# Kernel tuning notes

Hardware: AMD Instinct MI355X
Metric: run time of the kernel (lower is better)

The kernel has to match this reference:

```python
import jax, jax.numpy as jnp
import numpy as np

DIM = 512
HEADS = 8
FOCAL_LEVEL = 2  # depthwise kernel sizes: 3, 5 (focal_factor*k + focal_window)
LN_EPS = 1e-5


def _ln(x, w, b):
    m = jnp.mean(x, axis=-1, keepdims=True)
    v = jnp.var(x, axis=-1, keepdims=True)
    return (x - m) / jnp.sqrt(v + LN_EPS) * w + b


def _dwconv(x, w):
    # x: (B, C, H, W), w: (C, 1, k, k) depthwise, SAME padding (odd kernels)
    return jax.lax.conv_general_dilated(
        x, w, window_strides=(1, 1), padding='SAME',
        feature_group_count=x.shape[1],
        dimension_numbers=('NCHW', 'OIHW', 'NCHW'))


def setup_inputs() -> dict:
    key = jax.random.key(0)
    ks = jax.random.split(key, 16)
    B, Nl, H, W, d = 16, 512, 32, 32, DIM
    L = FOCAL_LEVEL
    p = lambda i, shape, s=0.02: (jax.random.normal(ks[i], shape, jnp.float32) * s)
    return {
        'latents': jax.random.normal(ks[0], (B, Nl, d), jnp.float32),
        'context': jax.random.normal(ks[1], (B, H * W, d), jnp.float32),
        'H': H, 'W': W,
        'norm_l_w': jnp.ones((d,), jnp.float32), 'norm_l_b': jnp.zeros((d,), jnp.float32),
        'norm_c_w': jnp.ones((d,), jnp.float32), 'norm_c_b': jnp.zeros((d,), jnp.float32),
        'norm2_w': jnp.ones((d,), jnp.float32), 'norm2_b': jnp.zeros((d,), jnp.float32),
        'Wq': p(2, (d, d)), 'Wk': p(3, (d, d)),
        'Wf': p(4, (d, d + L + 1)), 'bf': jnp.zeros((d + L + 1,), jnp.float32),
        'fk0': p(5, (d, 1, 3, 3), 0.1), 'fk1': p(6, (d, 1, 5, 5), 0.1),
        'h_w': p(7, (d, d)), 'h_b': jnp.zeros((d,), jnp.float32),
        'Wproj': p(8, (d, d)), 'bproj': jnp.zeros((d,), jnp.float32),
        'fc1_w': p(9, (d, 4 * d)), 'fc1_b': jnp.zeros((4 * d,), jnp.float32),
        'fc2_w': p(10, (4 * d, d)), 'fc2_b': jnp.zeros((d,), jnp.float32),
    }


def reference(latents, context, H, W,
              norm_l_w, norm_l_b, norm_c_w, norm_c_b, norm2_w, norm2_b,
              Wq, Wk, Wf, bf, fk0, fk1, h_w, h_b, Wproj, bproj,
              fc1_w, fc1_b, fc2_w, fc2_b):
    B, Nl, C = latents.shape
    Nc = context.shape[1]
    hd = C // HEADS
    scale = hd ** -0.5
    L = FOCAL_LEVEL
    gelu = lambda x: jax.nn.gelu(x, approximate=False)  # torch nn.GELU default

    xl = _ln(latents, norm_l_w, norm_l_b)
    xc = _ln(context, norm_c_w, norm_c_b)

    # cross attention scores
    q = (xl @ Wq).reshape(B, Nl, HEADS, hd)
    k = (xc @ Wk).reshape(B, Nc, HEADS, hd)
    attn = jax.nn.softmax(jnp.einsum('bqhd,bkhd->bhqk', q, k) * scale, axis=-1)

    # focal modulation on the context to build V
    f = (xc @ Wf + bf).reshape(B, H, W, C + L + 1).transpose(0, 3, 1, 2)  # (B, C+L+1, H, W)
    v_ctx = f[:, :C]
    gates = f[:, C:]
    acc = jnp.zeros_like(v_ctx)
    for l, w in enumerate((fk0, fk1)):  # sequential multi-scale depthwise convs
        v_ctx = gelu(_dwconv(v_ctx, w))
        acc = acc + v_ctx * gates[:, l:l + 1]
    g = gelu(jnp.mean(v_ctx, axis=(2, 3), keepdims=True))  # global branch
    acc = acc + g * gates[:, L:L + 1]

    # 1x1 conv modulator h
    mod = jnp.einsum('bihw,io->bohw', acc, h_w) + h_b[None, :, None, None]
    v = mod.reshape(B, C, Nc).transpose(0, 2, 1).reshape(B, Nc, HEADS, hd)

    y = jnp.einsum('bhqk,bkhd->bqhd', attn, v).reshape(B, Nl, C) @ Wproj + bproj
    latents = latents + y
    h2 = _ln(latents, norm2_w, norm2_b)
    latents = latents + (gelu(h2 @ fc1_w + fc1_b) @ fc2_w + fc2_b)
    return latents
```

## Files before the change

kernel.cpp:

```cpp
#include <hip/hip_runtime.h>
#include <hip/hip_bf16.h>
#include <math.h>

#define NB 16
#define NLAT 512
#define NCTX 1024
#define CD 512
#define NH 8
#define HD 64

typedef unsigned short ushort_t;
typedef __attribute__((ext_vector_type(8))) __bf16 bf16x8;
typedef __attribute__((ext_vector_type(8))) unsigned short u16x8;
typedef __attribute__((ext_vector_type(4))) unsigned short u16x4;
typedef __attribute__((ext_vector_type(4))) float f32x4;
typedef __attribute__((ext_vector_type(2))) unsigned int u32x2;

__device__ __forceinline__ float bf2f(unsigned short u) {
  return __uint_as_float(((unsigned int)u) << 16);
}
__device__ __forceinline__ unsigned short f2bf(float f) {
  unsigned int x = __float_as_uint(f);
  return (unsigned short)((x + 0x7fffu + ((x >> 16) & 1u)) >> 16);
}
__device__ __forceinline__ float gelu_f(float x) {
  return 0.5f * x * (1.f + erff(x * 0.70710678118654752f));
}

typedef const __attribute__((address_space(1))) unsigned int* gptr1;
typedef __attribute__((address_space(3))) unsigned int* lptr3;
__device__ __forceinline__ void gload16(const void* g, void* l) {
  __builtin_amdgcn_global_load_lds((gptr1)g, (lptr3)l, 16, 0, 0);
}
__device__ __forceinline__ u32x2 tr64(unsigned a) {
  u32x2 d;
  asm volatile("ds_read_b64_tr_b16 %0, %1" : "=v"(d) : "v"(a));
  return d;
}
__device__ __forceinline__ void gload16_asm(const void* g, unsigned lds_uniform_base) {
  unsigned sb = __builtin_amdgcn_readfirstlane(lds_uniform_base);
  asm volatile("s_mov_b32 m0, %0\n"
               "global_load_lds_dwordx4 %1, off"
               :: "s"(sb), "v"(g) : "memory");
}
template<int N> __device__ __forceinline__ void vmwait() {
  if constexpr (N == 0)       asm volatile("s_waitcnt vmcnt(0)" ::: "memory");
  else if constexpr (N == 2)  asm volatile("s_waitcnt vmcnt(2)" ::: "memory");
  else if constexpr (N == 3)  asm volatile("s_waitcnt vmcnt(3)" ::: "memory");
  else if constexpr (N == 4)  asm volatile("s_waitcnt vmcnt(4)" ::: "memory");
  else if constexpr (N == 6)  asm volatile("s_waitcnt vmcnt(6)" ::: "memory");
  else if constexpr (N == 8)  asm volatile("s_waitcnt vmcnt(8)" ::: "memory");
  else if constexpr (N == 9)  asm volatile("s_waitcnt vmcnt(9)" ::: "memory");
}

__global__ __launch_bounds__(256)
void wprep(const float* __restrict__ Wq, const float* __restrict__ Wk,
           const float* __restrict__ Wf, const float* __restrict__ hw_,
           const float* __restrict__ Wp, const float* __restrict__ f1,
           const float* __restrict__ f2, const float* __restrict__ bfv,
           ushort_t* __restrict__ WqT, ushort_t* __restrict__ WkT,
           ushort_t* __restrict__ WfT, ushort_t* __restrict__ hwT,
           ushort_t* __restrict__ WpT, ushort_t* __restrict__ fc1T,
           ushort_t* __restrict__ fc2T, float* __restrict__ biaskf) {
  int b = blockIdx.x;
  if (b >= 3344) {
    int i = threadIdx.x;
#pragma unroll
    for (int j = 0; j < 4; j++) {
      int idx = j * 256 + i;
      biaskf[idx] = (idx < 512) ? 0.f : bfv[idx - 512];
    }
    return;
  }
  const float* W; ushort_t* WT; int K, N, tile;
  if (b < 256)       { W = Wq;  WT = WqT;  K = 512;  N = 512;  tile = b; }
  else if (b < 512)  { W = Wk;  WT = WkT;  K = 512;  N = 512;  tile = b - 256; }
  else if (b < 784)  { W = Wf;  WT = WfT;  K = 512;  N = 515;  tile = b - 512; }
  else if (b < 1040) { W = hw_; WT = hwT;  K = 512;  N = 512;  tile = b - 784; }
  else if (b < 1296) { W = Wp;  WT = WpT;  K = 512;  N = 512;  tile = b - 1040; }
  else if (b < 2320) { W = f1;  WT = fc1T; K = 512;  N = 2048; tile = b - 1296; }
  else               { W = f2;  WT = fc2T; K = 2048; N = 512;  tile = b - 2320; }
  int Kt = K >> 5;
  int kb = (tile % Kt) * 32, nb = (tile / Kt) * 32;
  __shared__ float ts[32][33];
  int tx = threadIdx.x & 31, ty = threadIdx.x >> 5;
  for (int i = ty; i < 32; i += 8) {
    int k = kb + i, n = nb + tx;
    ts[i][tx] = (k < K && n < N) ? W[(size_t)k * N + n] : 0.f;
  }
  __syncthreads();
  for (int i = ty; i < 32; i += 8) {
    int n = nb + i, k = kb + tx;
    if (n < N && k < K) WT[(size_t)n * K + k] = f2bf(ts[tx][i]);
  }
}

__global__ __launch_bounds__(256)
void ln_kernel(const float* __restrict__ x, const float* __restrict__ gw,
               const float* __restrict__ gb, ushort_t* __restrict__ out, int nrows) {
  int row = blockIdx.x * 4 + (threadIdx.x >> 6);
  int lane = threadIdx.x & 63;
  const float4* xr = (const float4*)(x + (size_t)row * CD);
  float4 a = xr[lane * 2], b = xr[lane * 2 + 1];
  float s  = a.x + a.y + a.z + a.w + b.x + b.y + b.z + b.w;
  float s2 = a.x*a.x + a.y*a.y + a.z*a.z + a.w*a.w + b.x*b.x + b.y*b.y + b.z*b.z + b.w*b.w;
  for (int off = 32; off; off >>= 1) { s += __shfl_xor(s, off); s2 += __shfl_xor(s2, off); }
  float mean = s * (1.f / CD);
  float inv = rsqrtf(s2 * (1.f / CD) - mean * mean + 1e-5f);
  const float4* wv = (const float4*)gw;
  const float4* bv = (const float4*)gb;
  float4 w0 = wv[lane*2], w1 = wv[lane*2+1], c0 = bv[lane*2], c1 = bv[lane*2+1];
  u16x8 o;
  o[0] = f2bf((a.x - mean) * inv * w0.x + c0.x);
  o[1] = f2bf((a.y - mean) * inv * w0.y + c0.y);
  o[2] = f2bf((a.z - mean) * inv * w0.z + c0.z);
  o[3] = f2bf((a.w - mean) * inv * w0.w + c0.w);
  o[4] = f2bf((b.x - mean) * inv * w1.x + c1.x);
  o[5] = f2bf((b.y - mean) * inv * w1.y + c1.y);
  o[6] = f2bf((b.z - mean) * inv * w1.z + c1.z);
  o[7] = f2bf((b.w - mean) * inv * w1.w + c1.w);
  *(u16x8*)(out + (size_t)row * CD + lane * 8) = o;
  (void)nrows;
}

template<int BM, int BN, int ACT_GELU, int HAS_BIAS, int HAS_RES, int OUT_BF16>
__global__ __launch_bounds__(256)
void gemm9(const ushort_t* __restrict__ A, const ushort_t* __restrict__ BT,
           const float* __restrict__ bias, const float* __restrict__ res,
           void* __restrict__ outp, int N, int K) {
  constexpr int TM = BM / 2, FM = TM / 16;
  constexpr int TN = BN / 2, FN = TN / 16;
  constexpr int LA = BM / 64, LB = BN / 64, L = LA + LB;
  constexpr int SLOT = (BM + BN) * 32;
  __shared__ __attribute__((aligned(16))) ushort_t SH[3][SLOT];

  const int t = threadIdx.x;
  const int lane = t & 63;
  const int wv = t >> 6;
  const int wr = wv >> 1, wc = wv & 1;
  const int g = lane >> 4, l15 = lane & 15;
  const int xsw = (g ^ ((l15 >> 1) & 3)) * 8;
  const size_t m0 = (size_t)blockIdx.x * BM;
  const size_t n0 = (size_t)blockIdx.y * BN;
  const int nK = K >> 5;

  f32x4 acc[FM][FN] = {};

  const ushort_t* Abase = A + m0 * K;
  const ushort_t* Bbase = BT + n0 * K;
  const unsigned shb = (unsigned)(size_t)(lptr3)&SH[0][0];
  const unsigned wofs = (unsigned)wv * 1024;

  auto stage = [&](int s, int kt) {
    const unsigned sb = shb + (unsigned)s * (SLOT * 2);
    const ushort_t* As = Abase + (size_t)kt * 32;
#pragma unroll
    for (int i = 0; i < LA; i++) {
      int li = i * 256 + t;
      int sc = ((li & 3) ^ ((li >> 3) & 3)) * 8;
      gload16_asm(As + (size_t)(li >> 2) * K + sc, sb + (unsigned)i * 4096 + wofs);
    }
    const ushort_t* Bs = Bbase + (size_t)kt * 32;
#pragma unroll
    for (int i = 0; i < LB; i++) {
      int li = i * 256 + t;
      int sc = ((li & 3) ^ ((li >> 3) & 3)) * 8;
      gload16_asm(Bs + (size_t)(li >> 2) * K + sc, sb + (unsigned)(BM * 64) + (unsigned)i * 4096 + wofs);
    }
  };

  auto compute = [&](int s) {
    const ushort_t* base = &SH[0][0] + s * SLOT;
    const ushort_t* Ab = base + wr * TM * 32;
    const ushort_t* Bb = base + BM * 32 + wc * TN * 32;
    bf16x8 Bf[FN], Af[FM];
#pragma unroll
    for (int n = 0; n < FN; n++)
      Bf[n] = *(const bf16x8*)(Bb + (n * 16 + l15) * 32 + xsw);
#pragma unroll
    for (int m = 0; m < FM; m++)
      Af[m] = *(const bf16x8*)(Ab + (m * 16 + l15) * 32 + xsw);
    __builtin_amdgcn_s_setprio(1);
#pragma unroll
    for (int m = 0; m < FM; m++)
#pragma unroll
      for (int n = 0; n < FN; n++)
        acc[m][n] = __builtin_amdgcn_mfma_f32_16x16x32_bf16(Af[m], Bf[n], acc[m][n], 0, 0, 0);
    __builtin_amdgcn_s_setprio(0);
  };

  stage(0, 0); stage(1, 1);
  for (int kt = 0; kt < nK; kt++) {
    int s = kt % 3;
    if (kt + 2 < nK) { stage((kt + 2) % 3, kt + 2); vmwait<2 * L>(); }
    else if (kt + 1 < nK) vmwait<L>();
    else vmwait<0>();
    __builtin_amdgcn_s_barrier();
    __builtin_amdgcn_sched_barrier(0);
    compute(s);
    __builtin_amdgcn_sched_barrier(0);
    __builtin_amdgcn_s_barrier();
  }

  const int colb = (int)n0 + wc * TN;
  float bv[FN];
#pragma unroll
  for (int n = 0; n < FN; n++) bv[n] = HAS_BIAS ? bias[colb + n * 16 + l15] : 0.f;

  if (OUT_BF16) {
    constexpr int ES = TN + 8;
    ushort_t* ep = &SH[0][0] + wv * (TM * ES);
#pragma unroll
    for (int m = 0; m < FM; m++)
#pragma unroll
      for (int n = 0; n < FN; n++)
#pragma unroll
        for (int r = 0; r < 4; r++) {
          float v = acc[m][n][r] + bv[n];
          if (ACT_GELU) v = gelu_f(v);
          ep[(m * 16 + g * 4 + r) * ES + n * 16 + l15] = f2bf(v);
        }
    asm volatile("s_waitcnt lgkmcnt(0)" ::: "memory");
    __builtin_amdgcn_sched_barrier(0);
    const size_t gr0 = m0 + wr * TM;
#pragma unroll
    for (int c = 0; c < TM * TN / 512; c++) {
      int idx = c * 512 + lane * 8;
      int lr = idx / TN, col = idx % TN;
      u16x8 vvv = *(const u16x8*)&ep[lr * ES + col];
      *(u16x8*)((ushort_t*)outp + (gr0 + lr) * N + colb + col) = vvv;
    }
  } else {
    const int rowb = (int)m0 + wr * TM + g * 4;
#pragma unroll
    for (int n = 0; n < FN; n++) {
      int col = colb + n * 16 + l15;
#pragma unroll
      for (int m = 0; m < FM; m++) {
#pragma unroll
        for (int r = 0; r < 4; r++) {
          size_t idx = (size_t)(rowb + m * 16 + r) * N + col;
          float v = acc[m][n][r] + bv[n];
          if (ACT_GELU) v = gelu_f(v);
          if (HAS_RES) v += res[idx];
          ((float*)outp)[idx] = v;
        }
      }
    }
  }
}

__global__ __launch_bounds__(256)
void gates_kernel(const ushort_t* __restrict__ xc, const ushort_t* __restrict__ WfT,
                  const float* __restrict__ bfv, float* __restrict__ gates) {
  int row = blockIdx.x * 4 + (threadIdx.x >> 6);
  int lane = threadIdx.x & 63;
  u16x8 xv = *(const u16x8*)(xc + (size_t)row * CD + lane * 8);
  float xf[8];
#pragma unroll
  for (int e = 0; e < 8; e++) xf[e] = bf2f(xv[e]);
  float sl[3];
#pragma unroll
  for (int l = 0; l < 3; l++) {
    u16x8 wvv = *(const u16x8*)(WfT + (size_t)(CD + l) * CD + lane * 8);
    float d = 0.f;
#pragma unroll
    for (int e = 0; e < 8; e++) d += xf[e] * bf2f(wvv[e]);
    for (int off = 32; off; off >>= 1) d += __shfl_xor(d, off);
    sl[l] = d;
  }
  if (lane == 0) {
    int b = row >> 10, p = row & 1023;
#pragma unroll
    for (int l = 0; l < 3; l++) gates[((size_t)b * 3 + l) * 1024 + p] = sl[l] + bfv[CD + l];
  }
}

__global__ __launch_bounds__(256)
void tr_bf16(const ushort_t* __restrict__ in, ushort_t* __restrict__ out, int R, int C,
             int irs, size_t ibs, size_t obs) {
  __shared__ ushort_t tile[64][72];
  size_t ibase = (size_t)blockIdx.z * ibs;
  size_t obase = (size_t)blockIdx.z * obs;
  int r0 = blockIdx.x * 64, c0 = blockIdx.y * 64;
  int t = threadIdx.x;
#pragma unroll
  for (int j = 0; j < 2; j++) {
    int lin = j * 256 + t;
    int r = lin >> 3, cc = (lin & 7) * 8;
    u16x8 v = *(const u16x8*)(in + ibase + (size_t)(r0 + r) * irs + c0 + cc);
#pragma unroll
    for (int e = 0; e < 8; e++) tile[r][cc + e] = v[e];
  }
  __syncthreads();
#pragma unroll
  for (int j = 0; j < 2; j++) {
    int lin = j * 256 + t;
    int c = lin >> 3, rr = (lin & 7) * 8;
    u16x8 v;
#pragma unroll
    for (int e = 0; e < 8; e++) v[e] = tile[rr + e][c];
    *(u16x8*)(out + obase + (size_t)(c0 + c) * R + r0 + rr) = v;
  }
}

__global__ __launch_bounds__(256)
void focal_conv(const ushort_t* __restrict__ ft, const float* __restrict__ gates,
                const float* __restrict__ fk0, const float* __restrict__ fk1,
                ushort_t* __restrict__ accc) {
  int bc = blockIdx.x;
  int b = bc >> 9, c = bc & 511;
  __shared__ float xs[34][37];
  __shared__ float vs[38][41];
  __shared__ float w0s[9], w1s[25];
  __shared__ float red[4];
  const int t = threadIdx.x;
  const int hh = t >> 3;
  const int w0c = (t & 7) * 4;

  float* xz = &xs[0][0];
  float* vz = &vs[0][0];
#pragma unroll
  for (int i = 0; i < 5; i++) { int idx = t + i * 256; if (idx < 34 * 37) xz[idx] = 0.f; }
#pragma unroll
  for (int i = 0; i < 7; i++) { int idx = t + i * 256; if (idx < 38 * 41) vz[idx] = 0.f; }
  if (t < 9)  w0s[t] = fk0[c * 9 + t];
  if (t < 25) w1s[t] = fk1[c * 25 + t];

  u16x4 vin = *(const u16x4*)(ft + (size_t)bc * 1024 + t * 4);
  const float* g0 = gates + (size_t)b * 3 * 1024;
  float4 ga = *(const float4*)(g0 + t * 4);
  float4 gb = *(const float4*)(g0 + 1024 + t * 4);
  float4 gc = *(const float4*)(g0 + 2048 + t * 4);
  __syncthreads();
#pragma unroll
  for (int j = 0; j < 4; j++) xs[hh + 1][w0c + 1 + j] = bf2f(vin[j]);
  __syncthreads();

  float accv[4];
  const float* gav = (const float*)&ga;
  const float* gbv = (const float*)&gb;
  const float* gcv = (const float*)&gc;
#pragma unroll
  for (int j = 0; j < 4; j++) {
    int ww = w0c + j;
    float s = 0.f;
#pragma unroll
    for (int dh = 0; dh < 3; dh++)
#pragma unroll
      for (int dw = 0; dw < 3; dw++)
        s += xs[hh + dh][ww + dw] * w0s[dh * 3 + dw];
    float v1 = gelu_f(s);
    vs[hh + 2][ww + 2] = v1;
    accv[j] = v1 * gav[j];
  }
  __syncthreads();

  float psum = 0.f;
#pragma unroll
  for (int j = 0; j < 4; j++) {
    int ww = w0c + j;
    float s = 0.f;
#pragma unroll
    for (int dh = 0; dh < 5; dh++)
#pragma unroll
      for (int dw = 0; dw < 5; dw++)
        s += vs[hh + dh][ww + dw] * w1s[dh * 5 + dw];
    float v2 = gelu_f(s);
    psum += v2;
    accv[j] += v2 * gbv[j];
  }
  for (int off = 32; off; off >>= 1) psum += __shfl_xor(psum, off);
  if ((t & 63) == 0) red[t >> 6] = psum;
  __syncthreads();
  float g = gelu_f((red[0] + red[1] + red[2] + red[3]) * (1.f / 1024.f));
  u16x4 o;
#pragma unroll
  for (int j = 0; j < 4; j++) o[j] = f2bf(accv[j] + g * gcv[j]);
  *(u16x4*)(accc + (size_t)bc * 1024 + t * 4) = o;
}

__global__ __launch_bounds__(512)
void flash_attn(const ushort_t* __restrict__ Q, const ushort_t* __restrict__ Kk,
                const ushort_t* __restrict__ V, ushort_t* __restrict__ Y, int kstride) {
  const int wg = blockIdx.x;
  const int swz = (wg & 7) * 64 + (wg >> 3);
  const int q0 = (swz & 3) * 128;
  const int h = (swz >> 2) & 7;
  const int b = swz >> 5;
  const int t = threadIdx.x, lane = t & 63, w = t >> 6;
  const int g = lane >> 4, l15 = lane & 15;
  __shared__ __attribute__((aligned(16))) ushort_t Ks[2][4096];
  __shared__ __attribute__((aligned(16))) ushort_t Vs[2][4096];
  __shared__ __attribute__((aligned(16))) ushort_t Ps[8][1024];

  const size_t qbase = (((size_t)b * NLAT) + q0 + w * 16 + l15) * CD + h * HD;
  bf16x8 aq[2];
#pragma unroll
  for (int kk = 0; kk < 2; kk++) {
    u16x8 u = *(const u16x8*)(Q + qbase + kk * 32 + g * 8);
    u16x8 o;
#pragma unroll
    for (int e = 0; e < 8; e++) o[e] = f2bf(bf2f(u[e]) * 0.125f);
    aq[kk] = *(bf16x8*)&o;
  }

  f32x4 accO[4] = {};
  float lsum[4] = {0.f, 0.f, 0.f, 0.f};
  const ushort_t* Kb = Kk + ((size_t)b * NCTX) * kstride + h * HD;
  const ushort_t* Vb = V  + ((size_t)b * NCTX) * CD + h * HD;
  const int krow = t >> 3;
  const int kseg = 8 * ((t & 7) ^ (krow & 7));
  const int vrow = (t >> 1) & 63;
  const int vcol = (t >> 7) * 16 + (t & 1) * 8;

  auto stage = [&](int buf, int kv) {
    const int k0 = kv * 64;
    gload16(Kb + (size_t)(k0 + krow) * kstride + kseg, &Ks[buf][t * 8]);
    gload16(Vb + (size_t)(k0 + vrow) * CD + vcol, &Vs[buf][t * 8]);
  };

  const unsigned vsbase0 = (unsigned)(size_t)(lptr3)&Vs[0][0];
  const unsigned vsbase1 = (unsigned)(size_t)(lptr3)&Vs[1][0];
  char* psb = (char*)&Ps[w][0];

  stage(0, 0);
  __syncthreads();
  int cur = 0;
  for (int kv = 0; kv < 16; kv++) {
    if (kv < 15) stage(cur ^ 1, kv + 1);

    const char* ksb = (const char*)&Ks[cur][0];
    f32x4 accS[4] = {};
#pragma unroll
    for (int kk = 0; kk < 2; kk++) {
#pragma unroll
      for (int n = 0; n < 4; n++) {
        int rr = n * 16 + l15;
        bf16x8 bk = *(const bf16x8*)(ksb + rr * 128 + ((kk * 64 + g * 16) ^ ((rr & 7) << 4)));
        accS[n] = __builtin_amdgcn_mfma_f32_16x16x32_bf16(aq[kk], bk, accS[n], 0, 0, 0);
      }
    }

#pragma unroll
    for (int n = 0; n < 4; n++)
#pragma unroll
      for (int r = 0; r < 4; r++) {
        float p = __expf(accS[n][r]);
        accS[n][r] = p;
        lsum[r] += p;
      }

#pragma unroll
    for (int n = 0; n < 4; n++)
#pragma unroll
      for (int r = 0; r < 4; r++) {
        int row = g * 4 + r;
        int cb = (n * 16 + l15) * 2;
        *(ushort_t*)(psb + row * 128 + (cb ^ ((row & 7) << 4))) = f2bf(accS[n][r]);
      }
    asm volatile("s_waitcnt lgkmcnt(0)" ::: "memory");
    __builtin_amdgcn_sched_barrier(0);
    bf16x8 ap0 = *(const bf16x8*)(psb + l15 * 128 + (((g * 16)) ^ ((l15 & 7) << 4)));
    bf16x8 ap1 = *(const bf16x8*)(psb + l15 * 128 + ((64 + g * 16) ^ ((l15 & 7) << 4)));

    const unsigned vsb = (cur ? vsbase1 : vsbase0) + g * 128;
    union PKU { u32x2 d2[2]; bf16x8 v; };
    PKU pk[8];
#pragma unroll
    for (int n = 0; n < 4; n++) {
      unsigned a = vsb + n * 2048;
      pk[n * 2].d2[0]     = tr64(a);
      pk[n * 2].d2[1]     = tr64(a + 128);
      pk[n * 2 + 1].d2[0] = tr64(a + 1024);
      pk[n * 2 + 1].d2[1] = tr64(a + 1152);
    }
    asm volatile("s_waitcnt lgkmcnt(0)" ::: "memory");
    __builtin_amdgcn_sched_barrier(0);
#pragma unroll
    for (int n = 0; n < 4; n++) {
      accO[n] = __builtin_amdgcn_mfma_f32_16x16x32_bf16(ap0, pk[n * 2].v, accO[n], 0, 0, 0);
      accO[n] = __builtin_amdgcn_mfma_f32_16x16x32_bf16(ap1, pk[n * 2 + 1].v, accO[n], 0, 0, 0);
    }
    __syncthreads();
    cur ^= 1;
  }

#pragma unroll
  for (int r = 0; r < 4; r++) {
    float s = lsum[r];
    s += __shfl_xor(s, 1); s += __shfl_xor(s, 2);
    s += __shfl_xor(s, 4); s += __shfl_xor(s, 8);
    lsum[r] = 1.f / s;
  }
#pragma unroll
  for (int n = 0; n < 4; n++) {
#pragma unroll
    for (int r = 0; r < 4; r++) {
      size_t row = q0 + w * 16 + g * 4 + r;
      size_t col = h * HD + n * 16 + l15;
      Y[(((size_t)b * NLAT) + row) * CD + col] = f2bf(accO[n][r] * lsum[r]);
    }
  }
}

extern "C" void kernel_launch(void* const* d_in, const int* in_sizes, int n_in,
                              void* d_out, int out_size, void* d_ws, size_t ws_size,
                              hipStream_t stream) {
  const float* latents  = (const float*)d_in[0];
  const float* context  = (const float*)d_in[1];
  const float* norm_l_w = (const float*)d_in[4];
  const float* norm_l_b = (const float*)d_in[5];
  const float* norm_c_w = (const float*)d_in[6];
  const float* norm_c_b = (const float*)d_in[7];
  const float* norm2_w  = (const float*)d_in[8];
  const float* norm2_b  = (const float*)d_in[9];
  const float* Wq    = (const float*)d_in[10];
  const float* Wk    = (const float*)d_in[11];
  const float* Wf    = (const float*)d_in[12];
  const float* bfv   = (const float*)d_in[13];
  const float* fk0   = (const float*)d_in[14];
  const float* fk1   = (const float*)d_in[15];
  const float* h_w   = (const float*)d_in[16];
  const float* h_b   = (const float*)d_in[17];
  const float* Wproj = (const float*)d_in[18];
  const float* bproj = (const float*)d_in[19];
  const float* fc1_w = (const float*)d_in[20];
  const float* fc1_b = (const float*)d_in[21];
  const float* fc2_w = (const float*)d_in[22];
  const float* fc2_b = (const float*)d_in[23];

  char* ws = (char*)d_ws;
  const size_t MB = 1024ull * 1024ull;
  ushort_t* WqT  = (ushort_t*)(ws + 0 * MB);
  ushort_t* WkT  = (ushort_t*)(ws + 1 * MB);
  ushort_t* WfT  = (ushort_t*)(ws + 1 * MB + 524288);
  ushort_t* hwT  = (ushort_t*)(ws + 3 * MB);
  ushort_t* WpT  = (ushort_t*)(ws + 4 * MB);
  ushort_t* fc1T = (ushort_t*)(ws + 5 * MB);
  ushort_t* fc2T = (ushort_t*)(ws + 7 * MB);
  float*    biaskf = (float*)(ws + 9 * MB);
  ushort_t* xl    = (ushort_t*)(ws + 10 * MB);
  ushort_t* xc    = (ushort_t*)(ws + 18 * MB);
  ushort_t* qb    = (ushort_t*)(ws + 34 * MB);
  ushort_t* kf    = (ushort_t*)(ws + 42 * MB);
  float*    gates = (float*)   (ws + 74 * MB);
  ushort_t* ftp   = (ushort_t*)(ws + 75 * MB);
  ushort_t* accc  = (ushort_t*)(ws + 91 * MB);
  ushort_t* acct  = (ushort_t*)(ws + 18 * MB);
  ushort_t* vb    = (ushort_t*)(ws + 75 * MB);
  ushort_t* yb    = (ushort_t*)(ws + 10 * MB);
  float*    lat1  = (float*)   (ws + 18 * MB);
  ushort_t* h2    = (ushort_t*)(ws + 34 * MB);
  ushort_t* a1    = (ushort_t*)(ws + 42 * MB);

  dim3 b256(256), b512(512);
  wprep<<<dim3(3345), b256, 0, stream>>>(Wq, Wk, Wf, h_w, Wproj, fc1_w, fc2_w, bfv,
                                         WqT, WkT, WfT, hwT, WpT, fc1T, fc2T, biaskf);
  ln_kernel<<<dim3(2048), b256, 0, stream>>>(latents, norm_l_w, norm_l_b, xl, 8192);
  ln_kernel<<<dim3(4096), b256, 0, stream>>>(context, norm_c_w, norm_c_b, xc, 16384);
  gemm9<128,64, 0,0,0,1><<<dim3(64, 8),   b256, 0, stream>>>(xl, WqT, nullptr, nullptr, qb, 512, 512);
  gemm9<128,64, 0,1,0,1><<<dim3(128, 16), b256, 0, stream>>>(xc, WkT, biaskf, nullptr, kf, 1024, 512);
  gates_kernel<<<dim3(4096), b256, 0, stream>>>(xc, WfT, bfv, gates);
  tr_bf16<<<dim3(16, 8, 16), b256, 0, stream>>>(kf + 512, ftp, 1024, 512, 1024, (size_t)1024*1024, (size_t)512*1024);
  focal_conv<<<dim3(8192), b256, 0, stream>>>(ftp, gates, fk0, fk1, accc);
  tr_bf16<<<dim3(8, 16, 16), b256, 0, stream>>>(accc, acct, 512, 1024, 1024, (size_t)512*1024, (size_t)1024*512);
  gemm9<128,64, 0,1,0,1><<<dim3(128, 8), b256, 0, stream>>>(acct, hwT, h_b, nullptr, vb, 512, 512);
  flash_attn<<<dim3(512), b512, 0, stream>>>(qb, kf, vb, yb, 1024);
  gemm9<128,64, 0,1,1,0><<<dim3(64, 8), b256, 0, stream>>>(yb, WpT, bproj, latents, lat1, 512, 512);
  ln_kernel<<<dim3(2048), b256, 0, stream>>>(lat1, norm2_w, norm2_b, h2, 8192);
  gemm9<128,64, 1,1,0,1><<<dim3(64, 32), b256, 0, stream>>>(h2, fc1T, fc1_b, nullptr, a1, 2048, 512);
  gemm9<128,64, 0,1,1,0><<<dim3(64, 8),  b256, 0, stream>>>(a1, fc2T, fc2_b, lat1, d_out, 512, 2048);
  (void)in_sizes; (void)n_in; (void)out_size; (void)ws_size;
}
```

Before: 238.3 us.

## Switch GEMMs to 64x64 tiles with 1D grid and XCD-aware block remap

Replaces the templated 128x64 GEMM with a fixed 64x64-tile kernel launched on a 1D grid. Block IDs are remapped so that consecutive tiles are grouped per XCD (bid&7 striding), which should improve L2 locality across the eight chiplets. Smaller tiles double the block count, giving more occupancy and better load balance across CUs, at the cost of lower per-block operand reuse and more global/LDS traffic per FLOP. Each stage now issues a single A and B load per thread.

```diff
diff --git a/kernel.cpp b/kernel.cpp
--- a/kernel.cpp
+++ b/kernel.cpp
@@ -37,20 +37,17 @@
   asm volatile("ds_read_b64_tr_b16 %0, %1" : "=v"(d) : "v"(a));
   return d;
 }
-__device__ __forceinline__ void gload16_asm(const void* g, unsigned lds_uniform_base) {
-  unsigned sb = __builtin_amdgcn_readfirstlane(lds_uniform_base);
+__device__ __forceinline__ void gload16_s(const void* g, unsigned sbase) {
   asm volatile("s_mov_b32 m0, %0\n"
                "global_load_lds_dwordx4 %1, off"
-               :: "s"(sb), "v"(g) : "memory");
+               :: "s"(sbase), "v"(g) : "memory");
 }
 template<int N> __device__ __forceinline__ void vmwait() {
   if constexpr (N == 0)       asm volatile("s_waitcnt vmcnt(0)" ::: "memory");
   else if constexpr (N == 2)  asm volatile("s_waitcnt vmcnt(2)" ::: "memory");
-  else if constexpr (N == 3)  asm volatile("s_waitcnt vmcnt(3)" ::: "memory");
   else if constexpr (N == 4)  asm volatile("s_waitcnt vmcnt(4)" ::: "memory");
   else if constexpr (N == 6)  asm volatile("s_waitcnt vmcnt(6)" ::: "memory");
   else if constexpr (N == 8)  asm volatile("s_waitcnt vmcnt(8)" ::: "memory");
-  else if constexpr (N == 9)  asm volatile("s_waitcnt vmcnt(9)" ::: "memory");
 }
 
 __global__ __launch_bounds__(256)
@@ -123,16 +120,19 @@
   (void)nrows;
 }
 
-template<int BM, int BN, int ACT_GELU, int HAS_BIAS, int HAS_RES, int OUT_BF16>
+template<int ACT_GELU, int HAS_BIAS, int HAS_RES, int OUT_BF16>
 __global__ __launch_bounds__(256)
-void gemm9(const ushort_t* __restrict__ A, const ushort_t* __restrict__ BT,
-           const float* __restrict__ bias, const float* __restrict__ res,
-           void* __restrict__ outp, int N, int K) {
-  constexpr int TM = BM / 2, FM = TM / 16;
-  constexpr int TN = BN / 2, FN = TN / 16;
-  constexpr int LA = BM / 64, LB = BN / 64, L = LA + LB;
-  constexpr int SLOT = (BM + BN) * 32;
+void gemm11(const ushort_t* __restrict__ A, const ushort_t* __restrict__ BT,
+            const float* __restrict__ bias, const float* __restrict__ res,
+            void* __restrict__ outp, int N, int K, int nN) {
+  constexpr int SLOT = 4096;
   __shared__ __attribute__((aligned(16))) ushort_t SH[3][SLOT];
+
+  const int bid = blockIdx.x;
+  const int q = gridDim.x >> 3;
+  const int lin = (bid & 7) * q + (bid >> 3);
+  const size_t m0 = (size_t)(lin / nN) * 64;
+  const size_t n0 = (size_t)(lin % nN) * 64;
 
   const int t = threadIdx.x;
   const int lane = t & 63;
@@ -140,51 +140,40 @@
   const int wr = wv >> 1, wc = wv & 1;
   const int g = lane >> 4, l15 = lane & 15;
   const int xsw = (g ^ ((l15 >> 1) & 3)) * 8;
-  const size_t m0 = (size_t)blockIdx.x * BM;
-  const size_t n0 = (size_t)blockIdx.y * BN;
   const int nK = K >> 5;
 
-  f32x4 acc[FM][FN] = {};
+  f32x4 acc[2][2] = {};
 
   const ushort_t* Abase = A + m0 * K;
   const ushort_t* Bbase = BT + n0 * K;
-  const unsigned shb = (unsigned)(size_t)(lptr3)&SH[0][0];
-  const unsigned wofs = (unsigned)wv * 1024;
+  const unsigned m0b = __builtin_amdgcn_readfirstlane(
+      (unsigned)(size_t)(lptr3)&SH[0][0] + (unsigned)wv * 1024u);
+
+  const int srow = t >> 2;
+  const int ssc = ((t & 3) ^ ((t >> 3) & 3)) * 8;
 
   auto stage = [&](int s, int kt) {
-    const unsigned sb = shb + (unsigned)s * (SLOT * 2);
-    const ushort_t* As = Abase + (size_t)kt * 32;
-#pragma unroll
-    for (int i = 0; i < LA; i++) {
-      int li = i * 256 + t;
-      int sc = ((li & 3) ^ ((li >> 3) & 3)) * 8;
-      gload16_asm(As + (size_t)(li >> 2) * K + sc, sb + (unsigned)i * 4096 + wofs);
-    }
-    const ushort_t* Bs = Bbase + (size_t)kt * 32;
-#pragma unroll
-    for (int i = 0; i < LB; i++) {
-      int li = i * 256 + t;
-      int sc = ((li & 3) ^ ((li >> 3) & 3)) * 8;
-      gload16_asm(Bs + (size_t)(li >> 2) * K + sc, sb + (unsigned)(BM * 64) + (unsigned)i * 4096 + wofs);
-    }
+    const unsigned sb = m0b + (unsigned)s * 8192u;
+    gload16_s(Abase + (size_t)srow * K + (size_t)kt * 32 + ssc, sb);
+    gload16_s(Bbase + (size_t)srow * K + (size_t)kt * 32 + ssc, sb + 4096u);
   };
 
   auto compute = [&](int s) {
     const ushort_t* base = &SH[0][0] + s * SLOT;
-    const ushort_t* Ab = base + wr * TM * 32;
-    const ushort_t* Bb = base + BM * 32 + wc * TN * 32;
-    bf16x8 Bf[FN], Af[FM];
-#pragma unroll
-    for (int n = 0; n < FN; n++)
+    const ushort_t* Ab = base + wr * (32 * 32);
+    const ushort_t* Bb = base + 64 * 32 + wc * (32 * 32);
+    bf16x8 Bf[2], Af[2];
+#pragma unroll
+    for (int n = 0; n < 2; n++)
       Bf[n] = *(const bf16x8*)(Bb + (n * 16 + l15) * 32 + xsw);
 #pragma unroll
-    for (int m = 0; m < FM; m++)
+    for (int m = 0; m < 2; m++)
       Af[m] = *(const bf16x8*)(Ab + (m * 16 + l15) * 32 + xsw);
     __builtin_amdgcn_s_setprio(1);
 #pragma unroll
-    for (int m = 0; m < FM; m++)
-#pragma unroll
-      for (int n = 0; n < FN; n++)
+    for (int m = 0; m < 2; m++)
+#pragma unroll
+      for (int n = 0; n < 2; n++)
         acc[m][n] = __builtin_amdgcn_mfma_f32_16x16x32_bf16(Af[m], Bf[n], acc[m][n], 0, 0, 0);
     __builtin_amdgcn_s_setprio(0);
   };
@@ -192,8 +181,8 @@
   stage(0, 0); stage(1, 1);
   for (int kt = 0; kt < nK; kt++) {
     int s = kt % 3;
-    if (kt + 2 < nK) { stage((kt + 2) % 3, kt + 2); vmwait<2 * L>(); }
-    else if (kt + 1 < nK) vmwait<L>();
+    if (kt + 2 < nK) { stage((kt + 2) % 3, kt + 2); vmwait<4>(); }
+    else if (kt + 1 < nK) vmwait<2>();
     else vmwait<0>();
     __builtin_amdgcn_s_barrier();
     __builtin_amdgcn_sched_barrier(0);
@@ -202,18 +191,18 @@
     __builtin_amdgcn_s_barrier();
   }
 
-  const int colb = (int)n0 + wc * TN;
-  float bv[FN];
-#pragma unroll
-  for (int n = 0; n < FN; n++) bv[n] = HAS_BIAS ? bias[colb + n * 16 + l15] : 0.f;
+  const int colb = (int)n0 + wc * 32;
+  float bv[2];
+#pragma unroll
+  for (int n = 0; n < 2; n++) bv[n] = HAS_BIAS ? bias[colb + n * 16 + l15] : 0.f;
 
   if (OUT_BF16) {
-    constexpr int ES = TN + 8;
-    ushort_t* ep = &SH[0][0] + wv * (TM * ES);
-#pragma unroll
-    for (int m = 0; m < FM; m++)
-#pragma unroll
-      for (int n = 0; n < FN; n++)
+    constexpr int ES = 40;
+    ushort_t* ep = &SH[0][0] + wv * (32 * ES);
+#pragma unroll
+    for (int m = 0; m < 2; m++)
+#pragma unroll
+      for (int n = 0; n < 2; n++)
 #pragma unroll
         for (int r = 0; r < 4; r++) {
           float v = acc[m][n][r] + bv[n];
@@ -222,21 +211,21 @@
         }
     asm volatile("s_waitcnt lgkmcnt(0)" ::: "memory");
     __builtin_amdgcn_sched_barrier(0);
-    const size_t gr0 = m0 + wr * TM;
-#pragma unroll
-    for (int c = 0; c < TM * TN / 512; c++) {
+    const size_t gr0 = m0 + wr * 32;
+#pragma unroll
+    for (int c = 0; c < 2; c++) {
       int idx = c * 512 + lane * 8;
-      int lr = idx / TN, col = idx % TN;
+      int lr = idx >> 5, col = idx & 31;
       u16x8 vvv = *(const u16x8*)&ep[lr * ES + col];
       *(u16x8*)((ushort_t*)outp + (gr0 + lr) * N + colb + col) = vvv;
     }
   } else {
-    const int rowb = (int)m0 + wr * TM + g * 4;
-#pragma unroll
-    for (int n = 0; n < FN; n++) {
+    const int rowb = (int)m0 + wr * 32 + g * 4;
+#pragma unroll
+    for (int n = 0; n < 2; n++) {
       int col = colb + n * 16 + l15;
 #pragma unroll
-      for (int m = 0; m < FM; m++) {
+      for (int m = 0; m < 2; m++) {
 #pragma unroll
         for (int r = 0; r < 4; r++) {
           size_t idx = (size_t)(rowb + m * 16 + r) * N + col;
@@ -559,17 +548,17 @@
                                          WqT, WkT, WfT, hwT, WpT, fc1T, fc2T, biaskf);
   ln_kernel<<<dim3(2048), b256, 0, stream>>>(latents, norm_l_w, norm_l_b, xl, 8192);
   ln_kernel<<<dim3(4096), b256, 0, stream>>>(context, norm_c_w, norm_c_b, xc, 16384);
-  gemm9<128,64, 0,0,0,1><<<dim3(64, 8),   b256, 0, stream>>>(xl, WqT, nullptr, nullptr, qb, 512, 512);
-  gemm9<128,64, 0,1,0,1><<<dim3(128, 16), b256, 0, stream>>>(xc, WkT, biaskf, nullptr, kf, 1024, 512);
+  gemm11<0,0,0,1><<<dim3(1024), b256, 0, stream>>>(xl, WqT, nullptr, nullptr, qb, 512, 512, 8);
+  gemm11<0,1,0,1><<<dim3(4096), b256, 0, stream>>>(xc, WkT, biaskf, nullptr, kf, 1024, 512, 16);
   gates_kernel<<<dim3(4096), b256, 0, stream>>>(xc, WfT, bfv, gates);
   tr_bf16<<<dim3(16, 8, 16), b256, 0, stream>>>(kf + 512, ftp, 1024, 512, 1024, (size_t)1024*1024, (size_t)512*1024);
   focal_conv<<<dim3(8192), b256, 0, stream>>>(ftp, gates, fk0, fk1, accc);
   tr_bf16<<<dim3(8, 16, 16), b256, 0, stream>>>(accc, acct, 512, 1024, 1024, (size_t)512*1024, (size_t)1024*512);
-  gemm9<128,64, 0,1,0,1><<<dim3(128, 8), b256, 0, stream>>>(acct, hwT, h_b, nullptr, vb, 512, 512);
+  gemm11<0,1,0,1><<<dim3(2048), b256, 0, stream>>>(acct, hwT, h_b, nullptr, vb, 512, 512, 8);
   flash_attn<<<dim3(512), b512, 0, stream>>>(qb, kf, vb, yb, 1024);
-  gemm9<128,64, 0,1,1,0><<<dim3(64, 8), b256, 0, stream>>>(yb, WpT, bproj, latents, lat1, 512, 512);
+  gemm11<0,1,1,0><<<dim3(1024), b256, 0, stream>>>(yb, WpT, bproj, latents, lat1, 512, 512, 8);
   ln_kernel<<<dim3(2048), b256, 0, stream>>>(lat1, norm2_w, norm2_b, h2, 8192);
-  gemm9<128,64, 1,1,0,1><<<dim3(64, 32), b256, 0, stream>>>(h2, fc1T, fc1_b, nullptr, a1, 2048, 512);
-  gemm9<128,64, 0,1,1,0><<<dim3(64, 8),  b256, 0, stream>>>(a1, fc2T, fc2_b, lat1, d_out, 512, 2048);
+  gemm11<1,1,0,1><<<dim3(4096), b256, 0, stream>>>(h2, fc1T, fc1_b, nullptr, a1, 2048, 512, 32);
+  gemm11<0,1,1,0><<<dim3(1024), b256, 0, stream>>>(a1, fc2T, fc2_b, lat1, d_out, 512, 2048, 8);
   (void)in_sizes; (void)n_in; (void)out_size; (void)ws_size;
 }
```

New measurement: 259.5 us. 1.09x slower.
